# Kernel optimization log

Hardware: AMD Instinct MI355X
Metric: run time of the kernel (lower is better)

Reference implementation:

```python
import jax, jax.numpy as jnp
import numpy as np

N_NODES = 27
SRC = jnp.array([0,1,1,1,1,2,2,2,3,3,3,4,4,4,5,5,5,5,6,6,6,6,6,7,7,7,8,8,8,9,9,9,10,10,10,11,11,11,12,12,12,13,13,13,14,14,14,15,15,15,16,16,16,17,17,17,18,18,18,18,19,20,21,21,21,22,23,23,23,24,25,26], dtype=jnp.int32)
DST = jnp.array([1,0,2,4,6,1,3,7,2,4,24,1,3,5,4,6,17,19,1,5,7,8,10,2,6,23,6,9,16,8,10,13,6,9,11,10,12,23,11,13,21,9,12,14,13,15,20,14,16,18,8,15,17,5,16,18,15,17,25,26,5,14,12,22,23,21,7,11,21,3,18,18], dtype=jnp.int32)


def _conv2d(x, w, b):
    # x: [BN, Cin, H, W], w: [Cout, Cin, 3, 3] -> SAME padding conv
    y = jax.lax.conv_general_dilated(x, w, window_strides=(1, 1), padding='SAME',
                                     dimension_numbers=('NCHW', 'OIHW', 'NCHW'))
    return y + b[None, :, None, None]


def _block(h, w, b):
    # h: [B, N, Cin, H, W]; Conv2dMessage (conv -> scatter-add over edges) + LeakyReLU(0.2) + MaxPool2d(2)
    B, N, C, H, W = h.shape
    y = _conv2d(h.reshape(B * N, C, H, W), w, b).reshape(B, N, -1, H, W)
    # propagate with aggr='add': out[dst] += y[src]; isolated-in nodes become zero
    agg = jnp.zeros_like(y).at[:, DST].add(y[:, SRC])
    a = jax.nn.leaky_relu(agg, negative_slope=0.2)
    Co = a.shape[2]
    p = jax.lax.reduce_window(a.reshape(B * N, Co, H, W), -jnp.inf, jax.lax.max,
                              (1, 1, 2, 2), (1, 1, 2, 2), 'VALID')
    return p.reshape(B, N, Co, H // 2, W // 2)


def setup_inputs() -> dict:
    key = jax.random.key(0)
    ks = jax.random.split(key, 9)
    B, Cin, H, W = 32, 4, 64, 64
    x = jax.random.normal(ks[0], (B, Cin, H, W), dtype=jnp.float32)
    def kaiming(k, shape):
        fan_in = int(np.prod(shape[1:]))
        bound = float(np.sqrt(6.0 / fan_in))
        return jax.random.uniform(k, shape, jnp.float32, -bound, bound)
    w1 = kaiming(ks[1], (32, Cin, 3, 3)); b1 = jnp.zeros((32,), jnp.float32)
    w2 = kaiming(ks[2], (64, 32, 3, 3));  b2 = jnp.zeros((64,), jnp.float32)
    w3 = kaiming(ks[3], (128, 64, 3, 3)); b3 = jnp.zeros((128,), jnp.float32)
    wc = kaiming(ks[4], (1, 128));        bc = jnp.zeros((1,), jnp.float32)
    return {"x": x, "w1": w1, "b1": b1, "w2": w2, "b2": b2,
            "w3": w3, "b3": b3, "wc": wc, "bc": bc}


def reference(x, w1, b1, w2, b2, w3, b3, wc, bc):
    B = x.shape[0]
    # torch.tile(xi, (27,1,1,1)) vectorized over batch -> [B, 27, C, H, W]
    h = jnp.broadcast_to(x[:, None], (B, N_NODES) + x.shape[1:])
    h = _block(h, w1, b1)   # [B, 27, 32, 32, 32]
    h = _block(h, w2, b2)   # [B, 27, 64, 16, 16]
    h = _block(h, w3, b3)   # [B, 27, 128, 8, 8]
    feat = h.mean(axis=(3, 4))                 # AdaptiveAvgPool2d(1) + flatten -> [B, 27, 128]
    logits = jnp.einsum('bnc,oc->bno', feat, wc) + bc  # [B, 27, 1]
    return logits[:, 0, :]                     # classifier(xi)[0] per sample -> [B, 1]
```

## Files before the change

kernel.cpp:

```cpp
#include <hip/hip_runtime.h>


#define LRELU(v) fmaxf((v), 0.2f * (v))

#define P1H_ELEMS (32 * 32 * 34 * 36)
#define P2H_ELEMS (32 * 64 * 18 * 20)

typedef float vf2 __attribute__((ext_vector_type(2)));

__global__ __launch_bounds__(256, 4) void k1(const float* __restrict__ x,
                                             const float* __restrict__ w1,
                                             const float* __restrict__ b1,
                                             float* __restrict__ P1H,
                                             float* __restrict__ out) {
    __shared__ __align__(16) float obuf[1152];
    const int bx = blockIdx.x;
    const int b  = blockIdx.y;
    const int rb = bx & 3, cog = bx >> 2;
    const int t  = threadIdx.x;
    const int l = t & 63, wv = t >> 6;
    const int r = l >> 4, q = l & 15;
    const int row0 = 16 * rb + 4 * wv + r;

    if (bx == 0 && t == 0) out[b] = 0.f;

    for (int i = t; i < 288; i += 256)
        *(float4*)&obuf[4 * i] = make_float4(0.f, 0.f, 0.f, 0.f);
    __syncthreads();

    const bool cL = (q > 0), cR = (q < 15);
    const int colL = max(4 * q - 2, 0);
    const int colR = min(4 * q + 4, 62);

    vf2 acc[4][2];
    #pragma unroll
    for (int g = 0; g < 4; ++g) {
        float bias = b1[cog * 4 + g];
        acc[g][0] = (vf2){bias, bias};
        acc[g][1] = (vf2){bias, bias};
    }

    #pragma unroll
    for (int c = 0; c < 4; ++c) {
        float win[3][6];
        #pragma unroll
        for (int d = 0; d < 3; ++d) {
            int gr = row0 - 1 + d;
            bool v = (unsigned)gr < 64u;
            int grc = min(max(gr, 0), 63);
            const float* row = x + ((b * 4 + c) * 64 + grc) * 64;
            float2 L  = *(const float2*)(row + colL);
            float4 M  = *(const float4*)(row + 4 * q);
            float2 R2 = *(const float2*)(row + colR);
            win[d][0] = (v && cL) ? L.y : 0.f;
            win[d][1] = v ? M.x : 0.f;
            win[d][2] = v ? M.y : 0.f;
            win[d][3] = v ? M.z : 0.f;
            win[d][4] = v ? M.w : 0.f;
            win[d][5] = (v && cR) ? R2.x : 0.f;
        }
        vf2 wp[3][5];
        #pragma unroll
        for (int d = 0; d < 3; ++d)
            #pragma unroll
            for (int k = 0; k < 5; ++k)
                wp[d][k] = (vf2){win[d][k], win[d][k + 1]};
        #pragma unroll
        for (int g = 0; g < 4; ++g) {
            const float* wpt = &w1[((cog * 4 + g) * 4 + c) * 9];
            #pragma unroll
            for (int d = 0; d < 3; ++d)
                #pragma unroll
                for (int j = 0; j < 3; ++j) {
                    float w = wpt[3 * d + j];
                    acc[g][0] += w * wp[d][j];
                    acc[g][1] += w * wp[d][j + 2];
                }
        }
    }

    const int prow_l = 2 * wv + (r >> 1);
    #pragma unroll
    for (int g = 0; g < 4; ++g) {
        float m0 = fmaxf(LRELU(acc[g][0].x), LRELU(acc[g][0].y));
        float m1 = fmaxf(LRELU(acc[g][1].x), LRELU(acc[g][1].y));
        float p0 = fmaxf(m0, __shfl_xor(m0, 16));
        float p1 = fmaxf(m1, __shfl_xor(m1, 16));
        if ((r & 1) == 0) {
            obuf[(g * 8 + prow_l) * 36 + 2 * q + 1] = 12.f * p0;
            obuf[(g * 8 + prow_l) * 36 + 2 * q + 2] = 12.f * p1;
        }
    }
    __syncthreads();

    for (int i = t; i < 288; i += 256) {
        int co_l = i / 72, rem = i % 72, pr = rem / 9, cw = rem % 9;
        *(float4*)&P1H[((b * 32 + cog * 4 + co_l) * 34 + 8 * rb + pr + 1) * 36 + 4 * cw] =
            *(const float4*)&obuf[4 * i];
    }
    if (rb == 0 || rb == 3) {
        int h = rb ? 33 : 0;
        for (int i = t; i < 36; i += 256) {
            int co_l = i / 9, cw = i % 9;
            *(float4*)&P1H[((b * 32 + cog * 4 + co_l) * 34 + h) * 36 + 4 * cw] =
                make_float4(0.f, 0.f, 0.f, 0.f);
        }
    }
}

__global__ __launch_bounds__(256, 4) void k2(const float* __restrict__ P1H,
                                             const float* __restrict__ w2,
                                             const float* __restrict__ b2,
                                             float* __restrict__ p2H) {
    __shared__ __align__(16) float xin[6912];
    __shared__ __align__(16) float obuf[640];
    const int bx = blockIdx.x;
    const int b  = blockIdx.y;
    const int cog = bx >> 3, rs = bx & 7;
    const int c0  = cog * 16;
    const int t = threadIdx.x, l = t & 63;
    const int wvs = __builtin_amdgcn_readfirstlane(t >> 6);
    const int ql = l & 15, R = l >> 4;

    for (int i = t; i < 1728; i += 256) {
        int cin = i / 54, rem = i % 54, r = rem / 9, cw = rem % 9;
        *(float4*)&xin[cin * 216 + r * 36 + 4 * cw] =
            *(const float4*)&P1H[((b * 32 + cin) * 34 + rs * 4 + r) * 36 + 4 * cw];
    }
    for (int i = t; i < 160; i += 256)
        *(float4*)&obuf[4 * i] = make_float4(0.f, 0.f, 0.f, 0.f);
    __syncthreads();

    vf2 acc[16];
    #pragma unroll
    for (int co = 0; co < 16; ++co) {
        float bias = (wvs == 0) ? 4.f * b2[c0 + co] : 0.f;
        acc[co] = (vf2){bias, bias};
    }

    #pragma unroll 2
    for (int cl = 0; cl < 8; ++cl) {
        const int cin = wvs * 8 + cl;
        float win[3][4];
        #pragma unroll
        for (int d = 0; d < 3; ++d) {
            const float* xr = &xin[cin * 216 + (R + d) * 36 + 2 * ql];
            float2 a0 = *(const float2*)xr;
            float2 a1 = *(const float2*)(xr + 2);
            win[d][0] = a0.x; win[d][1] = a0.y; win[d][2] = a1.x; win[d][3] = a1.y;
        }
        vf2 wp[3][3];
        #pragma unroll
        for (int d = 0; d < 3; ++d)
            #pragma unroll
            for (int k = 0; k < 3; ++k)
                wp[d][k] = (vf2){win[d][k], win[d][k + 1]};
        const int wbase = __builtin_amdgcn_readfirstlane((c0 * 32 + cin) * 9);
        #pragma unroll
        for (int co = 0; co < 16; ++co) {
            const float* wg = w2 + wbase + co * 288;
            float wt[9];
            #pragma unroll
            for (int k = 0; k < 9; ++k) wt[k] = wg[k];
            #pragma unroll
            for (int d = 0; d < 3; ++d)
                #pragma unroll
                for (int j = 0; j < 3; ++j)
                    acc[co] += wt[3 * d + j] * wp[d][j];
        }
    }

    __syncthreads();
    if (wvs > 0) {
        float* cb = &xin[((wvs - 1) * 64 + l) * 36];
        #pragma unroll
        for (int g = 0; g < 8; ++g)
            *(float4*)&cb[4 * g] = make_float4(acc[2 * g].x, acc[2 * g].y,
                                               acc[2 * g + 1].x, acc[2 * g + 1].y);
    }
    __syncthreads();
    if (wvs == 0) {
        #pragma unroll
        for (int k = 0; k < 3; ++k) {
            const float* cb = &xin[(k * 64 + l) * 36];
            #pragma unroll
            for (int g = 0; g < 8; ++g) {
                float4 v = *(const float4*)&cb[4 * g];
                acc[2 * g].x += v.x;     acc[2 * g].y += v.y;
                acc[2 * g + 1].x += v.z; acc[2 * g + 1].y += v.w;
            }
        }
        #pragma unroll
        for (int co = 0; co < 16; ++co) {
            float m = fmaxf(LRELU(acc[co].x), LRELU(acc[co].y));
            float p = fmaxf(m, __shfl_xor(m, 16));
            if ((R & 1) == 0)
                obuf[(co * 2 + (R >> 1)) * 20 + ql + 1] = p;
        }
    }
    __syncthreads();

    for (int i = t; i < 160; i += 256) {
        int co = i / 10, rem = i % 10, pr = rem / 5, cw = rem % 5;
        *(float4*)&p2H[((b * 64 + c0 + co) * 18 + rs * 2 + 1 + pr) * 20 + 4 * cw] =
            *(const float4*)&obuf[4 * i];
    }
    if (rs == 0 || rs == 7) {
        int h2 = rs ? 17 : 0;
        for (int i = t; i < 80; i += 256) {
            int co = i / 5, cw = i % 5;
            *(float4*)&p2H[((b * 64 + c0 + co) * 18 + h2) * 20 + 4 * cw] =
                make_float4(0.f, 0.f, 0.f, 0.f);
        }
    }
}

__global__ __launch_bounds__(256, 4) void k3(const float* __restrict__ p2H,
                                             const float* __restrict__ w3,
                                             const float* __restrict__ b3,
                                             const float* __restrict__ wc,
                                             const float* __restrict__ bc,
                                             float* __restrict__ out) {
    __shared__ __align__(16) float xs[5760];
    const int cog = blockIdx.x;
    const int b   = blockIdx.y;
    const int c0  = cog * 4;
    const int t   = threadIdx.x, l = t & 63;
    const int wvs = __builtin_amdgcn_readfirstlane(t >> 6);
    const int r   = l >> 2, q = l & 3;

    vf2 acc[4][2];
    #pragma unroll
    for (int g = 0; g < 4; ++g) {
        float bias = (wvs == 0) ? b3[c0 + g] : 0.f;
        acc[g][0] = (vf2){bias, bias};
        acc[g][1] = (vf2){bias, bias};
    }

    for (int ch = 0; ch < 4; ++ch) {
        if (ch) __syncthreads();
        for (int i = t; i < 1440; i += 256) {
            int cin_l = i / 90, rem = i % 90;
            *(float4*)&xs[cin_l * 360 + 4 * rem] =
                *(const float4*)&p2H[(b * 64 + ch * 16 + cin_l) * 360 + 4 * rem];
        }
        __syncthreads();
        #pragma unroll
        for (int cl = 0; cl < 4; ++cl) {
            const int cin_l = wvs * 4 + cl;
            const int cin   = ch * 16 + cin_l;
            const float* pb = &xs[cin_l * 360 + r * 20 + 4 * q];
            float win[3][6];
            #pragma unroll
            for (int d = 0; d < 3; ++d) {
                float4 M  = *(const float4*)(pb + d * 20);
                float2 Rt = *(const float2*)(pb + d * 20 + 4);
                win[d][0] = M.x; win[d][1] = M.y; win[d][2] = M.z;
                win[d][3] = M.w; win[d][4] = Rt.x; win[d][5] = Rt.y;
            }
            vf2 wp[3][5];
            #pragma unroll
            for (int d = 0; d < 3; ++d)
                #pragma unroll
                for (int k = 0; k < 5; ++k)
                    wp[d][k] = (vf2){win[d][k], win[d][k + 1]};
            const int wbase = __builtin_amdgcn_readfirstlane((c0 * 64 + cin) * 9);
            #pragma unroll
            for (int g = 0; g < 4; ++g) {
                const float* wg = w3 + wbase + g * 576;
                float wt[9];
                #pragma unroll
                for (int k = 0; k < 9; ++k) wt[k] = wg[k];
                #pragma unroll
                for (int d = 0; d < 3; ++d)
                    #pragma unroll
                    for (int j = 0; j < 3; ++j) {
                        float w = wt[3 * d + j];
                        acc[g][0] += w * wp[d][j];
                        acc[g][1] += w * wp[d][j + 2];
                    }
            }
        }
    }

    __syncthreads();
    if (wvs > 0) {
        float* cb = &xs[((wvs - 1) * 64 + l) * 20];
        #pragma unroll
        for (int g = 0; g < 4; ++g)
            *(float4*)&cb[4 * g] =
                make_float4(acc[g][0].x, acc[g][0].y, acc[g][1].x, acc[g][1].y);
    }
    __syncthreads();

    if (wvs == 0) {
        #pragma unroll
        for (int k = 0; k < 3; ++k) {
            const float* cb = &xs[(k * 64 + l) * 20];
            #pragma unroll
            for (int g = 0; g < 4; ++g) {
                float4 v = *(const float4*)&cb[4 * g];
                acc[g][0].x += v.x; acc[g][0].y += v.y;
                acc[g][1].x += v.z; acc[g][1].y += v.w;
            }
        }
        float vsum = 0.f;
        #pragma unroll
        for (int g = 0; g < 4; ++g) {
            float m0 = fmaxf(LRELU(acc[g][0].x), LRELU(acc[g][0].y));
            float m1 = fmaxf(LRELU(acc[g][1].x), LRELU(acc[g][1].y));
            float pm0 = fmaxf(m0, __shfl_xor(m0, 4));
            float pm1 = fmaxf(m1, __shfl_xor(m1, 4));
            float contrib = ((r & 1) == 0) ? (pm0 + pm1) : 0.f;
            vsum += contrib * wc[c0 + g];
        }
        #pragma unroll
        for (int off = 32; off > 0; off >>= 1) vsum += __shfl_xor(vsum, off);
        if (l == 0) {
            float o = vsum * (1.f / 64.f);
            if (cog == 0) o += bc[0];
            atomicAdd(&out[b], o);
        }
    }
}

extern "C" void kernel_launch(void* const* d_in, const int* in_sizes, int n_in,
                              void* d_out, int out_size, void* d_ws, size_t ws_size,
                              hipStream_t stream) {
    const float* x  = (const float*)d_in[0];
    const float* w1 = (const float*)d_in[1];
    const float* b1 = (const float*)d_in[2];
    const float* w2 = (const float*)d_in[3];
    const float* b2 = (const float*)d_in[4];
    const float* w3 = (const float*)d_in[5];
    const float* b3 = (const float*)d_in[6];
    const float* wc = (const float*)d_in[7];
    const float* bc = (const float*)d_in[8];
    float* out = (float*)d_out;

    float* P1H = (float*)d_ws;
    float* p2H = P1H + P1H_ELEMS;

    k1<<<dim3(32, 32), 256, 0, stream>>>(x, w1, b1, P1H, out);
    k2<<<dim3(32, 32), 256, 0, stream>>>(P1H, w2, b2, p2H);
    k3<<<dim3(32, 32), 256, 0, stream>>>(p2H, w3, b3, wc, bc, out);
}
```

Before: 131.2 us.

## Halve per-block work in conv2/conv3 kernels to double grid and occupancy

k2 now gives each block two input rows (one pooled output row) and each thread one output pixel, replacing the two-pixel packed vf2 accumulators; the grid doubles to 64x32. k3 handles two output channels per block instead of four and streams input channels in eight chunks of eight. Both kernels shrink shared memory and raise launch_bounds to 8 blocks per CU, aiming for more parallelism and better latency hiding. The trade-off is more halo re-reads, more weight loads per FLOP, and giving up the packed two-wide FMA arithmetic.

```diff
diff --git a/kernel.cpp b/kernel.cpp
--- a/kernel.cpp
+++ b/kernel.cpp
@@ -108,53 +108,44 @@
     }
 }
 
-__global__ __launch_bounds__(256, 4) void k2(const float* __restrict__ P1H,
+__global__ __launch_bounds__(256, 8) void k2(const float* __restrict__ P1H,
                                              const float* __restrict__ w2,
                                              const float* __restrict__ b2,
                                              float* __restrict__ p2H) {
-    __shared__ __align__(16) float xin[6912];
-    __shared__ __align__(16) float obuf[640];
+    __shared__ __align__(16) float xin[4608];
+    __shared__ __align__(16) float obuf[320];
     const int bx = blockIdx.x;
     const int b  = blockIdx.y;
-    const int cog = bx >> 3, rs = bx & 7;
+    const int cog = bx >> 4, rs = bx & 15;
     const int c0  = cog * 16;
     const int t = threadIdx.x, l = t & 63;
     const int wvs = __builtin_amdgcn_readfirstlane(t >> 6);
-    const int ql = l & 15, R = l >> 4;
-
-    for (int i = t; i < 1728; i += 256) {
-        int cin = i / 54, rem = i % 54, r = rem / 9, cw = rem % 9;
-        *(float4*)&xin[cin * 216 + r * 36 + 4 * cw] =
-            *(const float4*)&P1H[((b * 32 + cin) * 34 + rs * 4 + r) * 36 + 4 * cw];
-    }
-    for (int i = t; i < 160; i += 256)
+    const int c  = l & 31;
+    const int rw = l >> 5;
+
+    for (int i = t; i < 1152; i += 256) {
+        int cin = i / 36, rem = i % 36, r = rem / 9, cw = rem % 9;
+        *(float4*)&xin[cin * 144 + r * 36 + 4 * cw] =
+            *(const float4*)&P1H[((b * 32 + cin) * 34 + rs * 2 + r) * 36 + 4 * cw];
+    }
+    for (int i = t; i < 80; i += 256)
         *(float4*)&obuf[4 * i] = make_float4(0.f, 0.f, 0.f, 0.f);
     __syncthreads();
 
-    vf2 acc[16];
-    #pragma unroll
-    for (int co = 0; co < 16; ++co) {
-        float bias = (wvs == 0) ? 4.f * b2[c0 + co] : 0.f;
-        acc[co] = (vf2){bias, bias};
-    }
+    float acc[16];
+    #pragma unroll
+    for (int co = 0; co < 16; ++co)
+        acc[co] = (wvs == 0) ? 4.f * b2[c0 + co] : 0.f;
 
     #pragma unroll 2
     for (int cl = 0; cl < 8; ++cl) {
         const int cin = wvs * 8 + cl;
-        float win[3][4];
+        float win[3][3];
         #pragma unroll
         for (int d = 0; d < 3; ++d) {
-            const float* xr = &xin[cin * 216 + (R + d) * 36 + 2 * ql];
-            float2 a0 = *(const float2*)xr;
-            float2 a1 = *(const float2*)(xr + 2);
-            win[d][0] = a0.x; win[d][1] = a0.y; win[d][2] = a1.x; win[d][3] = a1.y;
-        }
-        vf2 wp[3][3];
-        #pragma unroll
-        for (int d = 0; d < 3; ++d)
-            #pragma unroll
-            for (int k = 0; k < 3; ++k)
-                wp[d][k] = (vf2){win[d][k], win[d][k + 1]};
+            const float* xr = &xin[cin * 144 + (rw + d) * 36 + c];
+            win[d][0] = xr[0]; win[d][1] = xr[1]; win[d][2] = xr[2];
+        }
         const int wbase = __builtin_amdgcn_readfirstlane((c0 * 32 + cin) * 9);
         #pragma unroll
         for (int co = 0; co < 16; ++co) {
@@ -166,46 +157,47 @@
             for (int d = 0; d < 3; ++d)
                 #pragma unroll
                 for (int j = 0; j < 3; ++j)
-                    acc[co] += wt[3 * d + j] * wp[d][j];
+                    acc[co] += wt[3 * d + j] * win[d][j];
         }
     }
 
     __syncthreads();
     if (wvs > 0) {
-        float* cb = &xin[((wvs - 1) * 64 + l) * 36];
-        #pragma unroll
-        for (int g = 0; g < 8; ++g)
-            *(float4*)&cb[4 * g] = make_float4(acc[2 * g].x, acc[2 * g].y,
-                                               acc[2 * g + 1].x, acc[2 * g + 1].y);
+        float* cb = &xin[((wvs - 1) * 64 + l) * 20];
+        #pragma unroll
+        for (int g = 0; g < 4; ++g)
+            *(float4*)&cb[4 * g] = make_float4(acc[4 * g], acc[4 * g + 1],
+                                               acc[4 * g + 2], acc[4 * g + 3]);
     }
     __syncthreads();
     if (wvs == 0) {
         #pragma unroll
         for (int k = 0; k < 3; ++k) {
-            const float* cb = &xin[(k * 64 + l) * 36];
-            #pragma unroll
-            for (int g = 0; g < 8; ++g) {
+            const float* cb = &xin[(k * 64 + l) * 20];
+            #pragma unroll
+            for (int g = 0; g < 4; ++g) {
                 float4 v = *(const float4*)&cb[4 * g];
-                acc[2 * g].x += v.x;     acc[2 * g].y += v.y;
-                acc[2 * g + 1].x += v.z; acc[2 * g + 1].y += v.w;
+                acc[4 * g]     += v.x; acc[4 * g + 1] += v.y;
+                acc[4 * g + 2] += v.z; acc[4 * g + 3] += v.w;
             }
         }
         #pragma unroll
         for (int co = 0; co < 16; ++co) {
-            float m = fmaxf(LRELU(acc[co].x), LRELU(acc[co].y));
-            float p = fmaxf(m, __shfl_xor(m, 16));
-            if ((R & 1) == 0)
-                obuf[(co * 2 + (R >> 1)) * 20 + ql + 1] = p;
-        }
-    }
-    __syncthreads();
-
-    for (int i = t; i < 160; i += 256) {
-        int co = i / 10, rem = i % 10, pr = rem / 5, cw = rem % 5;
-        *(float4*)&p2H[((b * 64 + c0 + co) * 18 + rs * 2 + 1 + pr) * 20 + 4 * cw] =
+            float a  = LRELU(acc[co]);
+            float p1 = fmaxf(a, __shfl_xor(a, 1));
+            float p  = fmaxf(p1, __shfl_xor(p1, 32));
+            if (rw == 0 && (c & 1) == 0)
+                obuf[co * 20 + (c >> 1) + 1] = p;
+        }
+    }
+    __syncthreads();
+
+    for (int i = t; i < 80; i += 256) {
+        int co = i / 5, cw = i % 5;
+        *(float4*)&p2H[((b * 64 + c0 + co) * 18 + rs + 1) * 20 + 4 * cw] =
             *(const float4*)&obuf[4 * i];
     }
-    if (rs == 0 || rs == 7) {
+    if (rs == 0 || rs == 15) {
         int h2 = rs ? 17 : 0;
         for (int i = t; i < 80; i += 256) {
             int co = i / 5, cw = i % 5;
@@ -215,40 +207,39 @@
     }
 }
 
-__global__ __launch_bounds__(256, 4) void k3(const float* __restrict__ p2H,
+__global__ __launch_bounds__(256, 8) void k3(const float* __restrict__ p2H,
                                              const float* __restrict__ w3,
                                              const float* __restrict__ b3,
                                              const float* __restrict__ wc,
                                              const float* __restrict__ bc,
                                              float* __restrict__ out) {
-    __shared__ __align__(16) float xs[5760];
+    __shared__ __align__(16) float xs[3840];
     const int cog = blockIdx.x;
     const int b   = blockIdx.y;
-    const int c0  = cog * 4;
+    const int c0  = cog * 2;
     const int t   = threadIdx.x, l = t & 63;
     const int wvs = __builtin_amdgcn_readfirstlane(t >> 6);
     const int r   = l >> 2, q = l & 3;
 
-    vf2 acc[4][2];
-    #pragma unroll
-    for (int g = 0; g < 4; ++g) {
+    float acc[2][4];
+    #pragma unroll
+    for (int g = 0; g < 2; ++g) {
         float bias = (wvs == 0) ? b3[c0 + g] : 0.f;
-        acc[g][0] = (vf2){bias, bias};
-        acc[g][1] = (vf2){bias, bias};
-    }
-
-    for (int ch = 0; ch < 4; ++ch) {
+        acc[g][0] = bias; acc[g][1] = bias; acc[g][2] = bias; acc[g][3] = bias;
+    }
+
+    for (int ch = 0; ch < 8; ++ch) {
         if (ch) __syncthreads();
-        for (int i = t; i < 1440; i += 256) {
+        for (int i = t; i < 720; i += 256) {
             int cin_l = i / 90, rem = i % 90;
             *(float4*)&xs[cin_l * 360 + 4 * rem] =
-                *(const float4*)&p2H[(b * 64 + ch * 16 + cin_l) * 360 + 4 * rem];
+                *(const float4*)&p2H[(b * 64 + ch * 8 + cin_l) * 360 + 4 * rem];
         }
         __syncthreads();
         #pragma unroll
-        for (int cl = 0; cl < 4; ++cl) {
-            const int cin_l = wvs * 4 + cl;
-            const int cin   = ch * 16 + cin_l;
+        for (int cl = 0; cl < 2; ++cl) {
+            const int cin_l = wvs * 2 + cl;
+            const int cin   = ch * 8 + cin_l;
             const float* pb = &xs[cin_l * 360 + r * 20 + 4 * q];
             float win[3][6];
             #pragma unroll
@@ -258,15 +249,9 @@
                 win[d][0] = M.x; win[d][1] = M.y; win[d][2] = M.z;
                 win[d][3] = M.w; win[d][4] = Rt.x; win[d][5] = Rt.y;
             }
-            vf2 wp[3][5];
-            #pragma unroll
-            for (int d = 0; d < 3; ++d)
-                #pragma unroll
-                for (int k = 0; k < 5; ++k)
-                    wp[d][k] = (vf2){win[d][k], win[d][k + 1]};
             const int wbase = __builtin_amdgcn_readfirstlane((c0 * 64 + cin) * 9);
             #pragma unroll
-            for (int g = 0; g < 4; ++g) {
+            for (int g = 0; g < 2; ++g) {
                 const float* wg = w3 + wbase + g * 576;
                 float wt[9];
                 #pragma unroll
@@ -276,8 +261,10 @@
                     #pragma unroll
                     for (int j = 0; j < 3; ++j) {
                         float w = wt[3 * d + j];
-                        acc[g][0] += w * wp[d][j];
-                        acc[g][1] += w * wp[d][j + 2];
+                        acc[g][0] += w * win[d][j];
+                        acc[g][1] += w * win[d][j + 1];
+                        acc[g][2] += w * win[d][j + 2];
+                        acc[g][3] += w * win[d][j + 3];
                     }
             }
         }
@@ -287,9 +274,9 @@
     if (wvs > 0) {
         float* cb = &xs[((wvs - 1) * 64 + l) * 20];
         #pragma unroll
-        for (int g = 0; g < 4; ++g)
+        for (int g = 0; g < 2; ++g)
             *(float4*)&cb[4 * g] =
-                make_float4(acc[g][0].x, acc[g][0].y, acc[g][1].x, acc[g][1].y);
+                make_float4(acc[g][0], acc[g][1], acc[g][2], acc[g][3]);
     }
     __syncthreads();
 
@@ -298,17 +285,17 @@
         for (int k = 0; k < 3; ++k) {
             const float* cb = &xs[(k * 64 + l) * 20];
             #pragma unroll
-            for (int g = 0; g < 4; ++g) {
+            for (int g = 0; g < 2; ++g) {
                 float4 v = *(const float4*)&cb[4 * g];
-                acc[g][0].x += v.x; acc[g][0].y += v.y;
-                acc[g][1].x += v.z; acc[g][1].y += v.w;
+                acc[g][0] += v.x; acc[g][1] += v.y;
+                acc[g][2] += v.z; acc[g][3] += v.w;
             }
         }
         float vsum = 0.f;
         #pragma unroll
-        for (int g = 0; g < 4; ++g) {
-            float m0 = fmaxf(LRELU(acc[g][0].x), LRELU(acc[g][0].y));
-            float m1 = fmaxf(LRELU(acc[g][1].x), LRELU(acc[g][1].y));
+        for (int g = 0; g < 2; ++g) {
+            float m0 = fmaxf(LRELU(acc[g][0]), LRELU(acc[g][1]));
+            float m1 = fmaxf(LRELU(acc[g][2]), LRELU(acc[g][3]));
             float pm0 = fmaxf(m0, __shfl_xor(m0, 4));
             float pm1 = fmaxf(m1, __shfl_xor(m1, 4));
             float contrib = ((r & 1) == 0) ? (pm0 + pm1) : 0.f;
@@ -342,6 +329,6 @@
     float* p2H = P1H + P1H_ELEMS;
 
     k1<<<dim3(32, 32), 256, 0, stream>>>(x, w1, b1, P1H, out);
-    k2<<<dim3(32, 32), 256, 0, stream>>>(P1H, w2, b2, p2H);
-    k3<<<dim3(32, 32), 256, 0, stream>>>(p2H, w3, b3, wc, bc, out);
+    k2<<<dim3(64, 32), 256, 0, stream>>>(P1H, w2, b2, p2H);
+    k3<<<dim3(64, 32), 256, 0, stream>>>(p2H, w3, b3, wc, bc, out);
 }
```

Result: slower. 154.1 us (+17.5%).
